# Kernel tuning notes

Measured on AMD Instinct MI355X. Metric: run time of the kernel, lower is better.

The kernel has to match this reference:

```python
import jax, jax.numpy as jnp
import numpy as np

N_NODES = 50000
N_EDGES = 800000
IN_DIM = 128
OUT_DIM = 16
N_HEADS = 4
NEG_SLOPE = 0.01  # jax.nn.leaky_relu default, matches original


def setup_inputs() -> dict:
    key = jax.random.key(0)
    k = jax.random.split(key, 8)
    nodes = jax.random.normal(k[0], (N_NODES, IN_DIM), dtype=jnp.float32)
    edges = jax.random.uniform(k[1], (N_NODES, 1), dtype=jnp.float32)  # node-indexed edge attr (edges[senders] in source)
    senders = jax.random.randint(k[2], (N_EDGES,), 0, N_NODES, dtype=jnp.int32)
    receivers = jax.random.randint(k[3], (N_EDGES,), 0, N_NODES, dtype=jnp.int32)
    W = jax.random.normal(k[4], (N_HEADS * OUT_DIM, IN_DIM), dtype=jnp.float32) / np.sqrt(IN_DIM)
    b = jnp.zeros((N_HEADS * OUT_DIM,), dtype=jnp.float32)
    attn_W = jax.random.normal(k[5], (N_HEADS, 2 * OUT_DIM + 1), dtype=jnp.float32) / np.sqrt(2 * OUT_DIM + 1)
    attn_b = jnp.zeros((N_HEADS,), dtype=jnp.float32)
    return dict(nodes=nodes, edges=edges, senders=senders, receivers=receivers,
                W=W, b=b, attn_W=attn_W, attn_b=attn_b)


def _segment_softmax(logits, seg, num_segments):
    # logits: [E, H, 1]; softmax over edges sharing the same receiver
    m = jax.ops.segment_max(logits, seg, num_segments=num_segments)
    e = jnp.exp(logits - m[seg])
    s = jax.ops.segment_sum(e, seg, num_segments=num_segments)
    return e / s[seg]


def reference(nodes, edges, senders, receivers, W, b, attn_W, attn_b):
    n = nodes.shape[0]
    h = (nodes @ W.T + b).reshape(n, N_HEADS, OUT_DIM)       # [N, H, D]
    sent = h[senders]                                        # [E, H, D]
    recv = h[receivers]                                      # [E, H, D]
    sent_e = jnp.tile(edges[senders], (1, N_HEADS))[..., None]  # [E, H, 1]
    feat = jnp.concatenate([sent, recv, sent_e], axis=-1)    # [E, H, 2D+1]
    logits = (jnp.einsum('ehd,hd->eh', feat, attn_W) + attn_b)[..., None]  # [E, H, 1]
    logits = jax.nn.leaky_relu(logits, NEG_SLOPE)
    logits = logits * jnp.sum(sent_e)                        # scalar scaling as in source
    att = _segment_softmax(logits, receivers, n)             # [E, H, 1]
    msg = sent * att                                         # [E, H, D]
    out = jax.ops.segment_sum(msg, receivers, num_segments=n)  # [N, H, D]
    out = jax.nn.leaky_relu(out, NEG_SLOPE)                  # last=False branch
    return out.reshape(n, N_HEADS * OUT_DIM)
```

## Files before the change

kernel.cpp:

```cpp
#include <hip/hip_runtime.h>
#include <math.h>

#define N_NODES 50000
#define N_EDGES 800000
#define IN_DIM 128
#define OUT_DIM 16
#define N_HEADS 4
#define HID 64
#define AW_COLS 33
#define GN 16
#define GEMM_BLK ((N_NODES + GN - 1) / GN)
#define HE 16
#define HBLK ((N_EDGES + 256 * HE - 1) / (256 * HE))
#define MAXDEG 64

#define SMEM_DOUBLES 5120
#define SCR_OFF_D 4352

__global__ __launch_bounds__(256, 4) void gemm_hist(
    const float* __restrict__ nodes, const float* __restrict__ W,
    const float* __restrict__ b, const float* __restrict__ attn_W,
    const float* __restrict__ attn_b, const float* __restrict__ edges,
    float* __restrict__ h, double* __restrict__ z_src, double* __restrict__ z_dst,
    const int* __restrict__ senders, const int* __restrict__ receivers,
    int* __restrict__ counts, int* __restrict__ srt_padded,
    double* __restrict__ Ssum) {
    __shared__ double smem_d[SMEM_DOUBLES];
    float* sW = (float*)smem_d;
    float* sN = (float*)(smem_d + 4096);
    int t = threadIdx.x;

    if (blockIdx.x < HBLK) {
        double* red = smem_d;
        int base = blockIdx.x * 256 * HE + t;
        double sp = 0.0;
        #pragma unroll
        for (int j = 0; j < HE; ++j) {
            int e = base + j * 256;
            if (e < N_EDGES) {
                int r = receivers[e];
                int rank = atomicAdd(&counts[r], 1);
                if (rank < MAXDEG)
                    srt_padded[r * MAXDEG + rank] = senders[e];
                sp += (double)edges[senders[e]];
            }
        }
        red[t] = sp;
        __syncthreads();
        for (int off = 128; off > 0; off >>= 1) {
            if (t < off) red[t] += red[t + off];
            __syncthreads();
        }
        if (t == 0) atomicAdd(Ssum, red[0]);
    } else {
        for (int i4 = t; i4 < HID * IN_DIM / 4; i4 += 256) {
            int o = i4 >> 5, kq = i4 & 31;
            float4 v = ((const float4*)W)[i4];
            *(float4*)&sW[o * IN_DIM + (((kq + o) & 31) << 2)] = v;
        }
        int node0 = (blockIdx.x - HBLK) * GN;
        for (int i4 = t; i4 < GN * IN_DIM / 4; i4 += 256) {
            int ln = i4 >> 5, kq = i4 & 31;
            float4 v = ((const float4*)nodes)[(long long)(node0 + ln) * (IN_DIM / 4) + kq];
            *(float4*)&sN[ln * IN_DIM + (((kq + ln) & 31) << 2)] = v;
        }
        __syncthreads();

        int w = t >> 6, l = t & 63;
        int og = l & 15;
        int ng = l >> 4;
        int kbase = w * 8;

        double acc[4][4];
        #pragma unroll
        for (int j = 0; j < 4; ++j)
            #pragma unroll
            for (int i = 0; i < 4; ++i) acc[j][i] = 0.0;

        #pragma unroll
        for (int s = 0; s < 8; ++s) {
            int kq = kbase + s;
            float4 wq[4], xq[4];
            #pragma unroll
            for (int j = 0; j < 4; ++j) {
                int o = og + 16 * j;
                wq[j] = *(const float4*)&sW[o * IN_DIM + (((kq + o) & 31) << 2)];
            }
            #pragma unroll
            for (int i = 0; i < 4; ++i) {
                int n = ng + 4 * i;
                xq[i] = *(const float4*)&sN[n * IN_DIM + (((kq + n) & 31) << 2)];
            }
            #pragma unroll
            for (int j = 0; j < 4; ++j) {
                double wx = (double)wq[j].x, wy = (double)wq[j].y;
                double wz = (double)wq[j].z, ww = (double)wq[j].w;
                #pragma unroll
                for (int i = 0; i < 4; ++i) {
                    double nx = (double)xq[i].x, ny = (double)xq[i].y;
                    double nz = (double)xq[i].z, nw = (double)xq[i].w;
                    acc[j][i] += wx * nx; acc[j][i] += wy * ny;
                    acc[j][i] += wz * nz; acc[j][i] += ww * nw;
                }
            }
        }
        __syncthreads();

        double* scr = smem_d;
        float* h_lds = (float*)(smem_d + SCR_OFF_D);
        {
            double* dst = &scr[(w * 64 + l) * 17];
            #pragma unroll
            for (int j = 0; j < 4; ++j)
                #pragma unroll
                for (int i = 0; i < 4; ++i) dst[j * 4 + i] = acc[j][i];
        }
        __syncthreads();
        {
            int jw = w;
            double bj = (double)b[og + 16 * jw];
            #pragma unroll
            for (int i = 0; i < 4; ++i) {
                double sum = bj;
                sum += scr[(0 * 64 + l) * 17 + jw * 4 + i];
                sum += scr[(1 * 64 + l) * 17 + jw * 4 + i];
                sum += scr[(2 * 64 + l) * 17 + jw * 4 + i];
                sum += scr[(3 * 64 + l) * 17 + jw * 4 + i];
                h_lds[(ng + 4 * i) * HID + og + 16 * jw] = (float)sum;
            }
        }
        __syncthreads();

        int half = l >> 5;
        int o2 = l & 31;
        int nwbase = w * 4 + half * 2;
        int hd0 = o2 >> 4, d = o2 & 15;
        int hd1 = hd0 + 2;
        double aw00 = (double)attn_W[hd0 * AW_COLS + d];
        double aw01 = (double)attn_W[hd0 * AW_COLS + OUT_DIM + d];
        double aw10 = (double)attn_W[hd1 * AW_COLS + d];
        double aw11 = (double)attn_W[hd1 * AW_COLS + OUT_DIM + d];
        double wE0 = (double)attn_W[hd0 * AW_COLS + 2 * OUT_DIM];
        double wE1 = (double)attn_W[hd1 * AW_COLS + 2 * OUT_DIM];
        double bb0 = (double)attn_b[hd0], bb1 = (double)attn_b[hd1];
        #pragma unroll
        for (int j = 0; j < 2; ++j) {
            int nl = nwbase + j;
            int n = node0 + nl;
            float hf0 = h_lds[nl * HID + o2];
            float hf1 = h_lds[nl * HID + o2 + 32];
            double c00 = (double)hf0 * aw00;
            double c01 = (double)hf0 * aw01;
            double c10 = (double)hf1 * aw10;
            double c11 = (double)hf1 * aw11;
            #pragma unroll
            for (int k = 1; k <= 8; k <<= 1) {
                c00 += __shfl_xor(c00, k, 64);
                c01 += __shfl_xor(c01, k, 64);
                c10 += __shfl_xor(c10, k, 64);
                c11 += __shfl_xor(c11, k, 64);
            }
            if (d == 0) {
                double se = (double)edges[n];
                z_src[n * N_HEADS + hd0] = c00 + se * wE0;
                z_dst[n * N_HEADS + hd0] = c01 + bb0;
                z_src[n * N_HEADS + hd1] = c10 + se * wE1;
                z_dst[n * N_HEADS + hd1] = c11 + bb1;
            }
        }
        ((float4*)h)[(long long)node0 * (HID / 4) + t] = ((const float4*)h_lds)[t];
    }
}

__global__ __launch_bounds__(256, 8) void node_fused(
    const float* __restrict__ h, const double* __restrict__ z_src,
    const double* __restrict__ z_dst,
    const int* __restrict__ srt_padded, const int* __restrict__ counts,
    const double* __restrict__ Ssum, float* __restrict__ out) {
    int w = threadIdx.x >> 6;
    int lane = threadIdx.x & 63;
    int nA = blockIdx.x * 8 + w * 2;
    int nB = nA + 1;
    int hd = lane >> 4, q = lane & 15;

    int degA = counts[nA]; if (degA > MAXDEG) degA = MAXDEG;
    int degB = counts[nB]; if (degB > MAXDEG) degB = MAXDEG;
    double S = 4.0 * Ssum[0];
    double zdA = z_dst[nA * N_HEADS + hd];
    double zdB = z_dst[nB * N_HEADS + hd];

    int sA[4], sB[4];
    #pragma unroll
    for (int j = 0; j < 4; ++j) {
        int ei = q + 16 * j;
        sA[j] = (ei < degA) ? srt_padded[nA * MAXDEG + ei] : 0;
        sB[j] = (ei < degB) ? srt_padded[nB * MAXDEG + ei] : 0;
    }
    float yA[4], yB[4];
    #pragma unroll
    for (int j = 0; j < 4; ++j) {
        int ei = q + 16 * j;
        yA[j] = -INFINITY;
        yB[j] = -INFINITY;
        if (ei < degA) {
            double yy = z_src[sA[j] * N_HEADS + hd] + zdA;
            yy = yy > 0.0 ? yy : 0.01 * yy;
            yA[j] = (float)yy;
        }
        if (ei < degB) {
            double yy = z_src[sB[j] * N_HEADS + hd] + zdB;
            yy = yy > 0.0 ? yy : 0.01 * yy;
            yB[j] = (float)yy;
        }
    }
    float mA = fmaxf(fmaxf(yA[0], yA[1]), fmaxf(yA[2], yA[3]));
    float mB = fmaxf(fmaxf(yB[0], yB[1]), fmaxf(yB[2], yB[3]));
    #pragma unroll
    for (int k = 1; k <= 8; k <<= 1) {
        mA = fmaxf(mA, __shfl_xor(mA, k, 64));
        mB = fmaxf(mB, __shfl_xor(mB, k, 64));
    }
    float evA[4], evB[4];
    float dA = 0.f, dB = 0.f;
    #pragma unroll
    for (int j = 0; j < 4; ++j) {
        evA[j] = (yA[j] == -INFINITY) ? 0.f
               : __expf((float)(S * ((double)yA[j] - (double)mA)));
        dA += evA[j];
        evB[j] = (yB[j] == -INFINITY) ? 0.f
               : __expf((float)(S * ((double)yB[j] - (double)mB)));
        dB += evB[j];
    }
    #pragma unroll
    for (int k = 1; k <= 8; k <<= 1) {
        dA += __shfl_xor(dA, k, 64);
        dB += __shfl_xor(dB, k, 64);
    }
    float accA = 0.f;
    #pragma unroll
    for (int j = 0; j < 4; ++j) {
        unsigned long long mk = __ballot(evA[j] != 0.f);
        unsigned um = (unsigned)((mk | (mk >> 16) | (mk >> 32) | (mk >> 48)) & 0xFFFFull);
        while (um) {
            int qq = __builtin_ctz(um);
            um &= um - 1;
            int src = (lane & 48) | qq;
            float evv = __shfl(evA[j], src, 64);
            int sj = __shfl(sA[j], src, 64);
            if (evv != 0.f)
                accA = fmaf(evv, h[sj * HID + lane], accA);
        }
    }
    float accB = 0.f;
    #pragma unroll
    for (int j = 0; j < 4; ++j) {
        unsigned long long mk = __ballot(evB[j] != 0.f);
        unsigned um = (unsigned)((mk | (mk >> 16) | (mk >> 32) | (mk >> 48)) & 0xFFFFull);
        while (um) {
            int qq = __builtin_ctz(um);
            um &= um - 1;
            int src = (lane & 48) | qq;
            float evv = __shfl(evB[j], src, 64);
            int sj = __shfl(sB[j], src, 64);
            if (evv != 0.f)
                accB = fmaf(evv, h[sj * HID + lane], accB);
        }
    }
    float rA = (dA > 0.f) ? accA / dA : 0.f;
    float rB = (dB > 0.f) ? accB / dB : 0.f;
    out[nA * HID + lane] = rA > 0.f ? rA : 0.01f * rA;
    out[nB * HID + lane] = rB > 0.f ? rB : 0.01f * rB;
}

static inline char* ws_take(char*& p, size_t bytes) {
    char* cur = p;
    p += (bytes + 255) & ~(size_t)255;
    return cur;
}

extern "C" void kernel_launch(void* const* d_in, const int* in_sizes, int n_in,
                              void* d_out, int out_size, void* d_ws, size_t ws_size,
                              hipStream_t stream) {
    const float* nodes     = (const float*)d_in[0];
    const float* edges     = (const float*)d_in[1];
    const int*   senders   = (const int*)d_in[2];
    const int*   receivers = (const int*)d_in[3];
    const float* W         = (const float*)d_in[4];
    const float* b         = (const float*)d_in[5];
    const float* attn_W    = (const float*)d_in[6];
    const float* attn_b    = (const float*)d_in[7];
    float* out = (float*)d_out;

    char* p = (char*)d_ws;
    float*  h          = (float*)ws_take(p, sizeof(float) * N_NODES * HID);
    double* z_src      = (double*)ws_take(p, sizeof(double) * N_NODES * N_HEADS);
    double* z_dst      = (double*)ws_take(p, sizeof(double) * N_NODES * N_HEADS);
    int*    counts     = (int*)ws_take(p, sizeof(int) * N_NODES);
    char*   zpad       = ws_take(p, 256);
    double* Ssum       = (double*)zpad;
    int*    srt_padded = (int*)ws_take(p, sizeof(int) * (size_t)N_NODES * MAXDEG);

    hipMemsetAsync(counts, 0, ((sizeof(int) * N_NODES + 255) & ~(size_t)255) + 256, stream);

    gemm_hist<<<HBLK + GEMM_BLK, 256, 0, stream>>>(
        nodes, W, b, attn_W, attn_b, edges, h, z_src, z_dst,
        senders, receivers, counts, srt_padded, Ssum);
    node_fused<<<(N_NODES + 7) / 8, 256, 0, stream>>>(
        h, z_src, z_dst, srt_padded, counts, Ssum, out);
}
```

Before: 154.8 us.

## Split GEMM blocks across output-head halves to halve LDS and double block count

Each GEMM block now computes only 32 of the 64 output channels (two heads) for its 16 nodes, so the grid launches twice as many GEMM blocks. Shared memory per block shrinks from 40KB to 24KB and the per-thread accumulator array halves, which should raise occupancy and cut register pressure. In exchange, every node tile is loaded from global memory twice, and each block's attention-logit computation covers two heads instead of four.

```diff
diff --git a/kernel.cpp b/kernel.cpp
--- a/kernel.cpp
+++ b/kernel.cpp
@@ -14,8 +14,8 @@
 #define HBLK ((N_EDGES + 256 * HE - 1) / (256 * HE))
 #define MAXDEG 64
 
-#define SMEM_DOUBLES 5120
-#define SCR_OFF_D 4352
+#define SMEM_DOUBLES 3072
+#define SCR_OFF_D 2304
 
 __global__ __launch_bounds__(256, 4) void gemm_hist(
     const float* __restrict__ nodes, const float* __restrict__ W,
@@ -26,8 +26,8 @@
     int* __restrict__ counts, int* __restrict__ srt_padded,
     double* __restrict__ Ssum) {
     __shared__ double smem_d[SMEM_DOUBLES];
-    float* sW = (float*)smem_d;
-    float* sN = (float*)(smem_d + 4096);
+    float* sWh = (float*)smem_d;
+    float* sN = (float*)(smem_d + 2048);
     int t = threadIdx.x;
 
     if (blockIdx.x < HBLK) {
@@ -53,12 +53,15 @@
         }
         if (t == 0) atomicAdd(Ssum, red[0]);
     } else {
-        for (int i4 = t; i4 < HID * IN_DIM / 4; i4 += 256) {
+        int bidp = blockIdx.x - HBLK;
+        int hhalf = bidp & 1;
+        int node0 = (bidp >> 1) * GN;
+
+        for (int i4 = t; i4 < 32 * IN_DIM / 4; i4 += 256) {
             int o = i4 >> 5, kq = i4 & 31;
-            float4 v = ((const float4*)W)[i4];
-            *(float4*)&sW[o * IN_DIM + (((kq + o) & 31) << 2)] = v;
-        }
-        int node0 = (blockIdx.x - HBLK) * GN;
+            float4 v = ((const float4*)W)[(hhalf * 32 + o) * (IN_DIM / 4) + kq];
+            *(float4*)&sWh[o * IN_DIM + (((kq + o) & 31) << 2)] = v;
+        }
         for (int i4 = t; i4 < GN * IN_DIM / 4; i4 += 256) {
             int ln = i4 >> 5, kq = i4 & 31;
             float4 v = ((const float4*)nodes)[(long long)(node0 + ln) * (IN_DIM / 4) + kq];
@@ -71,20 +74,20 @@
         int ng = l >> 4;
         int kbase = w * 8;
 
-        double acc[4][4];
+        double acc[2][4];
         #pragma unroll
-        for (int j = 0; j < 4; ++j)
+        for (int j = 0; j < 2; ++j)
             #pragma unroll
             for (int i = 0; i < 4; ++i) acc[j][i] = 0.0;
 
         #pragma unroll
         for (int s = 0; s < 8; ++s) {
             int kq = kbase + s;
-            float4 wq[4], xq[4];
-            #pragma unroll
-            for (int j = 0; j < 4; ++j) {
+            float4 wq[2], xq[4];
+            #pragma unroll
+            for (int j = 0; j < 2; ++j) {
                 int o = og + 16 * j;
-                wq[j] = *(const float4*)&sW[o * IN_DIM + (((kq + o) & 31) << 2)];
+                wq[j] = *(const float4*)&sWh[o * IN_DIM + (((kq + o) & 31) << 2)];
             }
             #pragma unroll
             for (int i = 0; i < 4; ++i) {
@@ -92,7 +95,7 @@
                 xq[i] = *(const float4*)&sN[n * IN_DIM + (((kq + n) & 31) << 2)];
             }
             #pragma unroll
-            for (int j = 0; j < 4; ++j) {
+            for (int j = 0; j < 2; ++j) {
                 double wx = (double)wq[j].x, wy = (double)wq[j].y;
                 double wz = (double)wq[j].z, ww = (double)wq[j].w;
                 #pragma unroll
@@ -109,24 +112,24 @@
         double* scr = smem_d;
         float* h_lds = (float*)(smem_d + SCR_OFF_D);
         {
-            double* dst = &scr[(w * 64 + l) * 17];
-            #pragma unroll
-            for (int j = 0; j < 4; ++j)
+            double* dst = &scr[(w * 64 + l) * 9];
+            #pragma unroll
+            for (int j = 0; j < 2; ++j)
                 #pragma unroll
                 for (int i = 0; i < 4; ++i) dst[j * 4 + i] = acc[j][i];
         }
         __syncthreads();
-        {
+        if (w < 2) {
             int jw = w;
-            double bj = (double)b[og + 16 * jw];
+            double bj = (double)b[hhalf * 32 + og + 16 * jw];
             #pragma unroll
             for (int i = 0; i < 4; ++i) {
                 double sum = bj;
-                sum += scr[(0 * 64 + l) * 17 + jw * 4 + i];
-                sum += scr[(1 * 64 + l) * 17 + jw * 4 + i];
-                sum += scr[(2 * 64 + l) * 17 + jw * 4 + i];
-                sum += scr[(3 * 64 + l) * 17 + jw * 4 + i];
-                h_lds[(ng + 4 * i) * HID + og + 16 * jw] = (float)sum;
+                sum += scr[(0 * 64 + l) * 9 + jw * 4 + i];
+                sum += scr[(1 * 64 + l) * 9 + jw * 4 + i];
+                sum += scr[(2 * 64 + l) * 9 + jw * 4 + i];
+                sum += scr[(3 * 64 + l) * 9 + jw * 4 + i];
+                h_lds[(ng + 4 * i) * 32 + og + 16 * jw] = (float)sum;
             }
         }
         __syncthreads();
@@ -134,41 +137,35 @@
         int half = l >> 5;
         int o2 = l & 31;
         int nwbase = w * 4 + half * 2;
-        int hd0 = o2 >> 4, d = o2 & 15;
-        int hd1 = hd0 + 2;
-        double aw00 = (double)attn_W[hd0 * AW_COLS + d];
-        double aw01 = (double)attn_W[hd0 * AW_COLS + OUT_DIM + d];
-        double aw10 = (double)attn_W[hd1 * AW_COLS + d];
-        double aw11 = (double)attn_W[hd1 * AW_COLS + OUT_DIM + d];
-        double wE0 = (double)attn_W[hd0 * AW_COLS + 2 * OUT_DIM];
-        double wE1 = (double)attn_W[hd1 * AW_COLS + 2 * OUT_DIM];
-        double bb0 = (double)attn_b[hd0], bb1 = (double)attn_b[hd1];
+        int hdl = o2 >> 4, d = o2 & 15;
+        int hdg = hhalf * 2 + hdl;
+        double aw0 = (double)attn_W[hdg * AW_COLS + d];
+        double aw1 = (double)attn_W[hdg * AW_COLS + OUT_DIM + d];
+        double wE = (double)attn_W[hdg * AW_COLS + 2 * OUT_DIM];
+        double bbv = (double)attn_b[hdg];
         #pragma unroll
         for (int j = 0; j < 2; ++j) {
             int nl = nwbase + j;
             int n = node0 + nl;
-            float hf0 = h_lds[nl * HID + o2];
-            float hf1 = h_lds[nl * HID + o2 + 32];
-            double c00 = (double)hf0 * aw00;
-            double c01 = (double)hf0 * aw01;
-            double c10 = (double)hf1 * aw10;
-            double c11 = (double)hf1 * aw11;
+            float hf = h_lds[nl * 32 + o2];
+            double c0 = (double)hf * aw0;
+            double c1 = (double)hf * aw1;
             #pragma unroll
             for (int k = 1; k <= 8; k <<= 1) {
-                c00 += __shfl_xor(c00, k, 64);
-                c01 += __shfl_xor(c01, k, 64);
-                c10 += __shfl_xor(c10, k, 64);
-                c11 += __shfl_xor(c11, k, 64);
+                c0 += __shfl_xor(c0, k, 64);
+                c1 += __shfl_xor(c1, k, 64);
             }
             if (d == 0) {
                 double se = (double)edges[n];
-                z_src[n * N_HEADS + hd0] = c00 + se * wE0;
-                z_dst[n * N_HEADS + hd0] = c01 + bb0;
-                z_src[n * N_HEADS + hd1] = c10 + se * wE1;
-                z_dst[n * N_HEADS + hd1] = c11 + bb1;
-            }
-        }
-        ((float4*)h)[(long long)node0 * (HID / 4) + t] = ((const float4*)h_lds)[t];
+                z_src[n * N_HEADS + hdg] = c0 + se * wE;
+                z_dst[n * N_HEADS + hdg] = c1 + bbv;
+            }
+        }
+        if (t < 128) {
+            int node = t >> 3, c = t & 7;
+            ((float4*)h)[(long long)(node0 + node) * (HID / 4) + hhalf * 8 + c] =
+                ((const float4*)h_lds)[node * 8 + c];
+        }
     }
 }
 
@@ -302,7 +299,7 @@
 
     hipMemsetAsync(counts, 0, ((sizeof(int) * N_NODES + 255) & ~(size_t)255) + 256, stream);
 
-    gemm_hist<<<HBLK + GEMM_BLK, 256, 0, stream>>>(
+    gemm_hist<<<HBLK + 2 * GEMM_BLK, 256, 0, stream>>>(
         nodes, W, b, attn_W, attn_b, edges, h, z_src, z_dst,
         senders, receivers, counts, srt_padded, Ssum);
     node_fused<<<(N_NODES + 7) / 8, 256, 0, stream>>>(
```

Measured after the change: 155.7 us. No clear change (+0.6%).
